# Performance work log

Hardware: AMD Instinct MI355X
Metric: run time of the kernel (lower is better)

## Reference

```python
import jax, jax.numpy as jnp
import numpy as np

B, T, I, H, O = 4096, 512, 1, 64, 1


def setup_inputs() -> dict:
    key = jax.random.key(0)
    ks = jax.random.split(key, 7)
    s = 1.0 / np.sqrt(H)  # PyTorch default init scale
    return {
        "x": jax.random.normal(ks[0], (B, T, I), dtype=jnp.float32),
        "w_ih": jax.random.uniform(ks[1], (4 * H, I), jnp.float32, -s, s),
        "w_hh": jax.random.uniform(ks[2], (4 * H, H), jnp.float32, -s, s),
        "b_ih": jax.random.uniform(ks[3], (4 * H,), jnp.float32, -s, s),
        "b_hh": jax.random.uniform(ks[4], (4 * H,), jnp.float32, -s, s),
        "w_out": jax.random.uniform(ks[5], (O, H), jnp.float32, -s, s),
        "b_out": jax.random.uniform(ks[6], (O,), jnp.float32, -s, s),
    }


def reference(x, w_ih, w_hh, b_ih, b_hh, w_out, b_out):
    # x: [B, T, I]; PyTorch gate order in 4H dim is (i, f, g, o)
    b = b_ih + b_hh  # [4H]
    # precompute input projections for all timesteps: [T, B, 4H]
    xg = jnp.einsum("bti,gi->tbg", x, w_ih) + b

    def step(carry, xg_t):
        h, c = carry  # [B, H] each
        gates = xg_t + h @ w_hh.T  # [B, 4H]
        i, f, g, o = jnp.split(gates, 4, axis=-1)
        i = jax.nn.sigmoid(i)
        f = jax.nn.sigmoid(f)
        g = jnp.tanh(g)
        o = jax.nn.sigmoid(o)
        c = f * c + i * g
        h = o * jnp.tanh(c)
        return (h, c), None

    nb = x.shape[0]
    h0 = jnp.zeros((nb, w_hh.shape[1]), x.dtype)
    (h_T, _), _ = jax.lax.scan(step, (h0, h0), xg)
    # linear on last hidden state only (lstm_out[:, -1, :])
    return h_T @ w_out.T + b_out
```

## Files before the change

kernel.cpp:

```cpp
#include <hip/hip_runtime.h>


#define TT   512
#define MB   8
#define HP   72
#define BUFE (16 * HP)
#define SXP  10

#define L2E  1.4426950408889634f
#define L2E2 2.8853900817779268f

typedef _Float16 f16x8 __attribute__((ext_vector_type(8)));
typedef float    f32x4 __attribute__((ext_vector_type(4)));
typedef float    f32x2 __attribute__((ext_vector_type(2)));

#define MFMA16(a, b, c) __builtin_amdgcn_mfma_f32_16x16x32_f16((a), (b), (c), 0, 0, 0)

__device__ __forceinline__ float rcp_(float x)  { return __builtin_amdgcn_rcpf(x); }
__device__ __forceinline__ float exp2_(float x) { return __builtin_amdgcn_exp2f(x); }

__device__ __forceinline__ f16x8 cvt8s(const float4& u0, const float4& u1, float s) {
    f16x8 r;
    r[0] = (_Float16)(u0.x * s); r[1] = (_Float16)(u0.y * s);
    r[2] = (_Float16)(u0.z * s); r[3] = (_Float16)(u0.w * s);
    r[4] = (_Float16)(u1.x * s); r[5] = (_Float16)(u1.y * s);
    r[6] = (_Float16)(u1.z * s); r[7] = (_Float16)(u1.w * s);
    return r;
}

__global__ __launch_bounds__(256, 2) void lstm_mfma(
    const float* __restrict__ x,
    const float* __restrict__ w_ih,
    const float* __restrict__ w_hh,
    const float* __restrict__ b_ih,
    const float* __restrict__ b_hh,
    const float* __restrict__ w_out,
    const float* __restrict__ b_out,
    float* __restrict__ out)
{
    __shared__ __align__(16) float    sh_x[TT * SXP];
    __shared__ __align__(16) _Float16 hbuf[2 * BUFE];

    const int tid = threadIdx.x;
    const int w   = tid >> 6;
    const int L   = tid & 63;
    const int l16 = L & 15;
    const int h0  = L >> 4;
    const int b0  = blockIdx.x * MB;
    const int j   = 16 * w + l16;

    {
        const int q = tid >> 5;
        const int l = tid & 31;
        const float* xr = x + (size_t)(b0 + q) * TT;
        #pragma unroll
        for (int i = 0; i < TT / 32; ++i)
            sh_x[(l + 32 * i) * SXP + q] = xr[l + 32 * i];
    }
    for (int i = tid; i < 2 * BUFE; i += 256) hbuf[i] = (_Float16)0.0f;

    const float sc[4] = {-L2E, -L2E, L2E2, -L2E};
    f16x8 Bf[4][2];
    float wihv[4], biasv[4];
    #pragma unroll
    for (int s = 0; s < 4; ++s) {
        const int n = 64 * s + j;
        #pragma unroll
        for (int kt = 0; kt < 2; ++kt) {
            const float* p = w_hh + n * 64 + kt * 32 + h0 * 8;
            float4 u0 = *(const float4*)p;
            float4 u1 = *(const float4*)(p + 4);
            Bf[s][kt] = cvt8s(u0, u1, sc[s]);
        }
        wihv[s]  = w_ih[n] * sc[s];
        biasv[s] = (b_ih[n] + b_hh[n]) * sc[s];
    }

    const int aoff = l16 * HP + h0 * 8;
    const int xoff = 2 * h0;
    const int wr   = 4 * h0 * HP + j;

    f32x2 ccv = {0.0f, 0.0f};

    f32x4 ci[4];
    {
        const float2 x0 = *(const float2*)(sh_x + xoff);
        #pragma unroll
        for (int s = 0; s < 4; ++s) {
            ci[s][0] = fmaf(x0.x, wihv[s], biasv[s]);
            ci[s][1] = 0.0f;
            ci[s][2] = fmaf(x0.y, wihv[s], biasv[s]);
            ci[s][3] = 0.0f;
        }
    }

    __syncthreads();

    if (((blockIdx.x >> 8) ^ blockIdx.x) & 1) {
        __builtin_amdgcn_s_sleep(10);
    }

    auto step = [&](const _Float16* rb, _Float16* wb, int t) {
        f16x8 a0 = *(const f16x8*)(rb + aoff);
        f16x8 a1 = *(const f16x8*)(rb + aoff + 32);

        f32x4 acc[4];
        #pragma unroll
        for (int s = 0; s < 4; ++s)
            acc[s] = MFMA16(a1, Bf[s][1], MFMA16(a0, Bf[s][0], ci[s]));

        if (t + 1 < TT) {
            const float2 xn = *(const float2*)(sh_x + (t + 1) * SXP + xoff);
            const f32x2 xnv = {xn.x, xn.y};
            #pragma unroll
            for (int s = 0; s < 4; ++s) {
                f32x2 c2 = xnv * wihv[s] + biasv[s];
                ci[s][0] = c2[0];
                ci[s][2] = c2[1];
            }
        }

        f32x2 Ei = {exp2_(acc[0][0]), exp2_(acc[0][2])};
        f32x2 Ef = {exp2_(acc[1][0]), exp2_(acc[1][2])};
        f32x2 Eg = {exp2_(acc[2][0]), exp2_(acc[2][2])};
        f32x2 Eo = {exp2_(acc[3][0]), exp2_(acc[3][2])};
        f32x2 Di = Ei + 1.0f, Df = Ef + 1.0f, Dg = Eg + 1.0f, Do = Eo + 1.0f;

        f32x2 FG = Df * Dg, IG = Di * Dg, IF = Di * Df;
        f32x2 P  = Di * FG;
        float u  = rcp_(P[0] * P[1]);
        f32x2 inv = {u * P[1], u * P[0]};

        f32x2 si = FG * inv, sf = IG * inv;
        f32x2 tg = 1.0f - 2.0f * (IF * inv);
        ccv = sf * ccv + si * tg;

        f32x2 ca = ccv * L2E2;
        f32x2 Ec = {exp2_(fminf(ca[0], 30.0f)), exp2_(fminf(ca[1], 30.0f))};
        f32x2 Dc = Ec + 1.0f;
        f32x2 Q  = Do * Dc;
        float v  = rcp_(Q[0] * Q[1]);
        f32x2 iq = {v * Q[1], v * Q[0]};
        f32x2 hv = (iq * Dc) * (1.0f - 2.0f * (iq * Do));

        wb[wr]          = (_Float16)hv[0];
        wb[wr + 2 * HP] = (_Float16)hv[1];
        __syncthreads();
    };

    for (int t = 0; t < TT; t += 2) {
        step(hbuf,        hbuf + BUFE, t);
        step(hbuf + BUFE, hbuf,        t + 1);
    }

    const float wo = w_out[L];
    #pragma unroll
    for (int p = 0; p < 2; ++p) {
        const int q = 2 * w + p;
        float v = (float)hbuf[(2 * q) * HP + L] * wo;
        #pragma unroll
        for (int off = 32; off; off >>= 1) v += __shfl_down(v, off);
        if (L == 0) out[b0 + q] = v + b_out[0];
    }
}

extern "C" void kernel_launch(void* const* d_in, const int* in_sizes, int n_in,
                              void* d_out, int out_size, void* d_ws, size_t ws_size,
                              hipStream_t stream) {
    const float* x     = (const float*)d_in[0];
    const float* w_ih  = (const float*)d_in[1];
    const float* w_hh  = (const float*)d_in[2];
    const float* b_ih  = (const float*)d_in[3];
    const float* b_hh  = (const float*)d_in[4];
    const float* w_out = (const float*)d_in[5];
    const float* b_out = (const float*)d_in[6];
    float* out = (float*)d_out;

    lstm_mfma<<<4096 / MB, 256, 0, stream>>>(x, w_ih, w_hh, b_ih, b_hh,
                                             w_out, b_out, out);
}
```

Before: 305.5 us.

## Halve batch per block to 4 with 2-wave blocks and permuted hidden layout

Each block now handles 4 sequences with 128 threads (2 waves) instead of 8 with 256. Each wave does two 16-column MFMA tiles per gate and writes packed f16 pairs to the hidden buffer, so the hidden units are permuted and the recurrent weights and output weights are remapped to match. The change doubles the grid to increase per-CU parallelism and cut barrier width on the serial time loop, at the cost of more MFMAs per wave and less useful output per MFMA row. The start-up sleep stagger also becomes four phases instead of two.

```diff
diff --git a/kernel.cpp b/kernel.cpp
--- a/kernel.cpp
+++ b/kernel.cpp
@@ -2,15 +2,16 @@
 
 
 #define TT   512
-#define MB   8
+#define MB   4
 #define HP   72
 #define BUFE (16 * HP)
-#define SXP  10
+#define SXP  5
 
 #define L2E  1.4426950408889634f
 #define L2E2 2.8853900817779268f
 
 typedef _Float16 f16x8 __attribute__((ext_vector_type(8)));
+typedef _Float16 f16x2 __attribute__((ext_vector_type(2)));
 typedef float    f32x4 __attribute__((ext_vector_type(4)));
 typedef float    f32x2 __attribute__((ext_vector_type(2)));
 
@@ -19,16 +20,7 @@
 __device__ __forceinline__ float rcp_(float x)  { return __builtin_amdgcn_rcpf(x); }
 __device__ __forceinline__ float exp2_(float x) { return __builtin_amdgcn_exp2f(x); }
 
-__device__ __forceinline__ f16x8 cvt8s(const float4& u0, const float4& u1, float s) {
-    f16x8 r;
-    r[0] = (_Float16)(u0.x * s); r[1] = (_Float16)(u0.y * s);
-    r[2] = (_Float16)(u0.z * s); r[3] = (_Float16)(u0.w * s);
-    r[4] = (_Float16)(u1.x * s); r[5] = (_Float16)(u1.y * s);
-    r[6] = (_Float16)(u1.z * s); r[7] = (_Float16)(u1.w * s);
-    return r;
-}
-
-__global__ __launch_bounds__(256, 2) void lstm_mfma(
+__global__ __launch_bounds__(128, 2) void lstm_mfma(
     const float* __restrict__ x,
     const float* __restrict__ w_ih,
     const float* __restrict__ w_hh,
@@ -47,7 +39,6 @@
     const int l16 = L & 15;
     const int h0  = L >> 4;
     const int b0  = blockIdx.x * MB;
-    const int j   = 16 * w + l16;
 
     {
         const int q = tid >> 5;
@@ -57,73 +48,83 @@
         for (int i = 0; i < TT / 32; ++i)
             sh_x[(l + 32 * i) * SXP + q] = xr[l + 32 * i];
     }
-    for (int i = tid; i < 2 * BUFE; i += 256) hbuf[i] = (_Float16)0.0f;
+    for (int i = tid; i < 2 * BUFE; i += 128) hbuf[i] = (_Float16)0.0f;
 
     const float sc[4] = {-L2E, -L2E, L2E2, -L2E};
-    f16x8 Bf[4][2];
-    float wihv[4], biasv[4];
+    f16x8 Bf[4][2][2];
+    float wihv[4][2], biasv[4][2];
     #pragma unroll
     for (int s = 0; s < 4; ++s) {
-        const int n = 64 * s + j;
         #pragma unroll
-        for (int kt = 0; kt < 2; ++kt) {
-            const float* p = w_hh + n * 64 + kt * 32 + h0 * 8;
-            float4 u0 = *(const float4*)p;
-            float4 u1 = *(const float4*)(p + 4);
-            Bf[s][kt] = cvt8s(u0, u1, sc[s]);
+        for (int t = 0; t < 2; ++t) {
+            const int n = 64 * s + 32 * w + 16 * t + l16;
+            #pragma unroll
+            for (int kc = 0; kc < 2; ++kc) {
+                f16x8 f;
+                #pragma unroll
+                for (int i = 0; i < 8; ++i) {
+                    const int sk = 8 * h0 + 32 * kc + i;
+                    const int u  = 32 * (sk >> 5) + ((sk & 31) >> 1)
+                                 + 16 * (sk & 1);
+                    f[i] = (_Float16)(w_hh[n * 64 + u] * sc[s]);
+                }
+                Bf[s][t][kc] = f;
+            }
+            wihv[s][t]  = w_ih[n] * sc[s];
+            biasv[s][t] = (b_ih[n] + b_hh[n]) * sc[s];
         }
-        wihv[s]  = w_ih[n] * sc[s];
-        biasv[s] = (b_ih[n] + b_hh[n]) * sc[s];
     }
 
-    const int aoff = l16 * HP + h0 * 8;
-    const int xoff = 2 * h0;
-    const int wr   = 4 * h0 * HP + j;
+    const int aoff  = l16 * HP + 8 * h0;
+    const int wslot = 4 * h0 * HP + 32 * w + 2 * l16;
 
     f32x2 ccv = {0.0f, 0.0f};
 
-    f32x4 ci[4];
+    f32x4 ci[4][2];
     {
-        const float2 x0 = *(const float2*)(sh_x + xoff);
+        const float x0 = sh_x[h0];
         #pragma unroll
-        for (int s = 0; s < 4; ++s) {
-            ci[s][0] = fmaf(x0.x, wihv[s], biasv[s]);
-            ci[s][1] = 0.0f;
-            ci[s][2] = fmaf(x0.y, wihv[s], biasv[s]);
-            ci[s][3] = 0.0f;
-        }
+        for (int s = 0; s < 4; ++s)
+            #pragma unroll
+            for (int t = 0; t < 2; ++t) {
+                ci[s][t][0] = fmaf(x0, wihv[s][t], biasv[s][t]);
+                ci[s][t][1] = 0.0f; ci[s][t][2] = 0.0f; ci[s][t][3] = 0.0f;
+            }
     }
 
     __syncthreads();
 
-    if (((blockIdx.x >> 8) ^ blockIdx.x) & 1) {
-        __builtin_amdgcn_s_sleep(10);
+    {
+        const int ph = (blockIdx.x >> 8) & 3;
+        if      (ph == 1) __builtin_amdgcn_s_sleep(4);
+        else if (ph == 2) __builtin_amdgcn_s_sleep(8);
+        else if (ph == 3) __builtin_amdgcn_s_sleep(12);
     }
 
     auto step = [&](const _Float16* rb, _Float16* wb, int t) {
         f16x8 a0 = *(const f16x8*)(rb + aoff);
         f16x8 a1 = *(const f16x8*)(rb + aoff + 32);
 
-        f32x4 acc[4];
+        f32x4 acc[4][2];
         #pragma unroll
         for (int s = 0; s < 4; ++s)
-            acc[s] = MFMA16(a1, Bf[s][1], MFMA16(a0, Bf[s][0], ci[s]));
+            #pragma unroll
+            for (int u = 0; u < 2; ++u)
+                acc[s][u] = MFMA16(a1, Bf[s][u][1], MFMA16(a0, Bf[s][u][0], ci[s][u]));
 
         if (t + 1 < TT) {
-            const float2 xn = *(const float2*)(sh_x + (t + 1) * SXP + xoff);
-            const f32x2 xnv = {xn.x, xn.y};
+            const float xn = sh_x[(t + 1) * SXP + h0];
             #pragma unroll
             for (int s = 0; s < 4; ++s) {
-                f32x2 c2 = xnv * wihv[s] + biasv[s];
-                ci[s][0] = c2[0];
-                ci[s][2] = c2[1];
+                ci[s][0][0] = fmaf(xn, wihv[s][0], biasv[s][0]);
+                ci[s][1][0] = fmaf(xn, wihv[s][1], biasv[s][1]);
             }
         }
 
-        f32x2 Ei = {exp2_(acc[0][0]), exp2_(acc[0][2])};
-        f32x2 Ef = {exp2_(acc[1][0]), exp2_(acc[1][2])};
-        f32x2 Eg = {exp2_(acc[2][0]), exp2_(acc[2][2])};
-        f32x2 Eo = {exp2_(acc[3][0]), exp2_(acc[3][2])};
+        f32x2 Ei = {exp2_(acc[0][0][0]), exp2_(acc[0][1][0])};
+        f32x2 Ef = {exp2_(acc[1][0][0]), exp2_(acc[1][1][0])};
+        f32x2 Eg = {exp2_(acc[2][0][0]), exp2_(acc[2][1][0])};
+        f32x2 Eo = {exp2_(acc[3][0][0]), exp2_(acc[3][1][0])};
         f32x2 Di = Ei + 1.0f, Df = Ef + 1.0f, Dg = Eg + 1.0f, Do = Eo + 1.0f;
 
         f32x2 FG = Df * Dg, IG = Di * Dg, IF = Di * Df;
@@ -143,8 +144,10 @@
         f32x2 iq = {v * Q[1], v * Q[0]};
         f32x2 hv = (iq * Dc) * (1.0f - 2.0f * (iq * Do));
 
-        wb[wr]          = (_Float16)hv[0];
-        wb[wr + 2 * HP] = (_Float16)hv[1];
+        f16x2 hp;
+        hp[0] = (_Float16)hv[0];
+        hp[1] = (_Float16)hv[1];
+        *(f16x2*)(wb + wslot) = hp;
         __syncthreads();
     };
 
@@ -153,11 +156,12 @@
         step(hbuf + BUFE, hbuf,        t + 1);
     }
 
-    const float wo = w_out[L];
+    const int   uL = 32 * (L >> 5) + ((L & 31) >> 1) + 16 * (L & 1);
+    const float wo = w_out[uL];
     #pragma unroll
     for (int p = 0; p < 2; ++p) {
         const int q = 2 * w + p;
-        float v = (float)hbuf[(2 * q) * HP + L] * wo;
+        float v = (float)hbuf[(4 * q) * HP + L] * wo;
         #pragma unroll
         for (int off = 32; off; off >>= 1) v += __shfl_down(v, off);
         if (L == 0) out[b0 + q] = v + b_out[0];
@@ -176,6 +180,6 @@
     const float* b_out = (const float*)d_in[6];
     float* out = (float*)d_out;
 
-    lstm_mfma<<<4096 / MB, 256, 0, stream>>>(x, w_ih, w_hh, b_ih, b_hh,
+    lstm_mfma<<<4096 / MB, 128, 0, stream>>>(x, w_ih, w_hh, b_ih, b_hh,
                                              w_out, b_out, out);
 }
```

After: 342.0 us. 1.12x slower.
